# Performance work log

Hardware: AMD Instinct MI355X
Metric: run time of the kernel (lower is better)

The kernel has to match this reference:

```python
import jax, jax.numpy as jnp
import numpy as np

TOP_K = 2


def setup_inputs() -> dict:
    key = jax.random.key(0)
    ks = jax.random.split(key, 5)
    B, S, H, E, I = 2, 1024, 1024, 16, 1024
    scale = 1.0 / np.sqrt(H)
    return {
        "hidden_states": jax.random.normal(ks[0], (B, S, H), dtype=jnp.float32),
        "router_w": jax.random.normal(ks[1], (E, H), dtype=jnp.float32) * scale,   # nn.Linear(H,E).weight
        "gate_w": jax.random.normal(ks[2], (E, I, H), dtype=jnp.float32) * scale,  # per-expert Linear(H,I).weight
        "up_w": jax.random.normal(ks[3], (E, I, H), dtype=jnp.float32) * scale,
        "down_w": jax.random.normal(ks[4], (E, H, I), dtype=jnp.float32) * (1.0 / np.sqrt(I)),
    }


def reference(hidden_states, router_w, gate_w, up_w, down_w):
    orig_shape = hidden_states.shape
    x = hidden_states.reshape(-1, orig_shape[-1])  # [T, H]
    T = x.shape[0]
    E = router_w.shape[0]

    # Router: sigmoid -> top-k -> normalize
    logits = jnp.einsum("th,eh->te", x, router_w)           # [T, E]
    scores = jax.nn.sigmoid(logits)
    weights, indices = jax.lax.top_k(scores, TOP_K)         # [T, K]
    weights = weights / (weights.sum(axis=-1, keepdims=True) + 1e-20)

    # Dense per-token-per-expert combine weight (0 for unrouted pairs) ==
    # exact math of the torch gather/index_add loop.
    w_full = jnp.zeros((T, E), dtype=x.dtype).at[
        jnp.arange(T)[:, None], indices
    ].add(weights)                                          # [T, E]

    # Expert MLPs (SwiGLU) computed for all experts, zero-weighted combine.
    g = jax.nn.silu(jnp.einsum("th,eih->tei", x, gate_w))   # [T, E, I]
    u = jnp.einsum("th,eih->tei", x, up_w)                  # [T, E, I]
    out = jnp.einsum("te,tei,ehi->th", w_full, g * u, down_w)  # [T, H]
    return out.reshape(orig_shape)
```

## Files before the change

### kernel.cpp

```cpp
#include <hip/hip_runtime.h>
#include <stdint.h>

#define T_TOK 2048
#define H_DIM 1024
#define E_NUM 16
#define I_DIM 1024
#define TOTAL_ROWS (2 * T_TOK)
#define CPAD 16

typedef short bf16x8 __attribute__((ext_vector_type(8)));
typedef float f32x4 __attribute__((ext_vector_type(4)));

__device__ __forceinline__ void async_copy16(const void* g, void* l) {
  __builtin_amdgcn_global_load_lds(
      (const __attribute__((address_space(1))) void*)g,
      (__attribute__((address_space(3))) void*)l, 16, 0, 0);
}

__device__ __forceinline__ uint32_t f2bf(float f) {
  uint32_t u = __float_as_uint(f);
  return (u + 0x7FFFu + ((u >> 16) & 1u)) >> 16;
}
__device__ __forceinline__ uint32_t pk2bf(float lo, float hi) {
  return f2bf(lo) | (f2bf(hi) << 16);
}

__device__ __forceinline__ void stage8(const float* g, uint16_t* l) {
  float4 v0 = *(const float4*)g;
  float4 v1 = *(const float4*)(g + 4);
  uint4 p;
  p.x = pk2bf(v0.x, v0.y);
  p.y = pk2bf(v0.z, v0.w);
  p.z = pk2bf(v1.x, v1.y);
  p.w = pk2bf(v1.z, v1.w);
  *(uint4*)l = p;
}

__global__ __launch_bounds__(256) void router_kernel(
    const float* __restrict__ x, const float* __restrict__ rw,
    uint16_t* __restrict__ xbf, int* __restrict__ counts,
    int* __restrict__ tokens, float* __restrict__ wts) {
  const int t = blockIdx.x * 4 + (threadIdx.x >> 6);
  const int lane = threadIdx.x & 63;

  float4 xv[4];
  float acc[E_NUM];
#pragma unroll
  for (int e = 0; e < E_NUM; ++e) acc[e] = 0.f;

#pragma unroll
  for (int rep = 0; rep < 4; ++rep) {
    const int h0 = rep * 256 + lane * 4;
    xv[rep] = *(const float4*)(x + (size_t)t * H_DIM + h0);
    uint2 p;
    p.x = pk2bf(xv[rep].x, xv[rep].y);
    p.y = pk2bf(xv[rep].z, xv[rep].w);
    *(uint2*)(xbf + (size_t)t * H_DIM + h0) = p;
  }

#pragma unroll
  for (int e = 0; e < E_NUM; ++e) {
#pragma unroll
    for (int rep = 0; rep < 4; ++rep) {
      const float4 rv = *(const float4*)(rw + (size_t)e * H_DIM + rep * 256 + lane * 4);
      acc[e] += xv[rep].x * rv.x + xv[rep].y * rv.y + xv[rep].z * rv.z +
                xv[rep].w * rv.w;
    }
  }

#pragma unroll
  for (int e = 0; e < E_NUM; ++e) {
    float v = acc[e];
#pragma unroll
    for (int off = 32; off > 0; off >>= 1) v += __shfl_xor(v, off);
    acc[e] = v;
  }

  if (lane < 2) {
    float s[E_NUM];
#pragma unroll
    for (int e = 0; e < E_NUM; ++e) s[e] = 1.f / (1.f + expf(-acc[e]));
    int i1 = 0;
    float v1 = s[0];
#pragma unroll
    for (int e = 1; e < E_NUM; ++e)
      if (s[e] > v1) { v1 = s[e]; i1 = e; }
    int i2 = -1;
    float v2 = -1.f;
#pragma unroll
    for (int e = 0; e < E_NUM; ++e)
      if (e != i1 && s[e] > v2) { v2 = s[e]; i2 = e; }
    const float inv = 1.f / (v1 + v2 + 1e-20f);
    const int pe = (lane == 0) ? i1 : i2;
    const float pw = ((lane == 0) ? v1 : v2) * inv;
    const int slot = atomicAdd(&counts[pe * CPAD], 1);
    tokens[pe * T_TOK + slot] = t;
    wts[pe * T_TOK + slot] = pw;
  }
}

__global__ void offsets_kernel(const int* __restrict__ counts,
                               int* __restrict__ offsets) {
  if (threadIdx.x == 0) {
    int a = 0;
    for (int e = 0; e < E_NUM; ++e) {
      offsets[e] = a;
      a += counts[e * CPAD];
    }
    offsets[E_NUM] = a;
  }
}


__global__ __launch_bounds__(256, 4) void gemm1_kernel(
    const uint16_t* __restrict__ xbf, const float* __restrict__ gate,
    const float* __restrict__ up, const int* __restrict__ counts,
    const int* __restrict__ offsets, const int* __restrict__ tokens,
    const float* __restrict__ wts, uint16_t* __restrict__ hbuf) {
  const int e = blockIdx.z;
  const int count = counts[e * CPAD];
  const int m0 = blockIdx.y * 64;
  if (m0 >= count) return;
  const int n0 = blockIdx.x * 64;

  __shared__ __align__(16) uint16_t As[64 * 64];
  __shared__ __align__(16) uint16_t Bgs[64 * 64];
  __shared__ __align__(16) uint16_t Bus[64 * 64];
  __shared__ int tok_s[64];
  __shared__ float wt_s[64];

  const int tid = threadIdx.x;
  if (tid < 64) {
    const int slot = m0 + tid;
    int tk = 0;
    float w = 0.f;
    if (slot < count) {
      tk = tokens[e * T_TOK + slot];
      w = wts[e * T_TOK + slot];
    }
    tok_s[tid] = tk;
    wt_s[tid] = w;
  }
  __syncthreads();

  const int c0 = tid, c1 = tid + 256;
  const int m_a0 = c0 >> 3, m_a1 = c1 >> 3;
  const int kq0 = (c0 & 7) ^ (m_a0 & 7);
  const int kq1 = (c1 & 7) ^ (m_a1 & 7);

  const uint16_t* a_g0 = xbf + (size_t)tok_s[m_a0] * H_DIM + kq0 * 8;
  const uint16_t* a_g1 = xbf + (size_t)tok_s[m_a1] * H_DIM + kq1 * 8;
  uint16_t* a_l0 = As + c0 * 8;
  uint16_t* a_l1 = As + c1 * 8;

  const float* g_g0 = gate + ((size_t)e * I_DIM + n0 + m_a0) * H_DIM + kq0 * 8;
  const float* g_g1 = gate + ((size_t)e * I_DIM + n0 + m_a1) * H_DIM + kq1 * 8;
  const float* u_g0 = up + ((size_t)e * I_DIM + n0 + m_a0) * H_DIM + kq0 * 8;
  const float* u_g1 = up + ((size_t)e * I_DIM + n0 + m_a1) * H_DIM + kq1 * 8;
  uint16_t* bg_l0 = Bgs + c0 * 8;
  uint16_t* bg_l1 = Bgs + c1 * 8;
  uint16_t* bu_l0 = Bus + c0 * 8;
  uint16_t* bu_l1 = Bus + c1 * 8;

  const int wave = tid >> 6, lane = tid & 63;
  const int wm = (wave & 1) * 32, wn = (wave >> 1) * 32;
  const int lc = lane & 15, lq = lane >> 4;
  const int l7 = lc & 7;

  f32x4 accg[2][2], accu[2][2];
  const f32x4 zero4 = {0.f, 0.f, 0.f, 0.f};
#pragma unroll
  for (int i = 0; i < 2; ++i)
#pragma unroll
    for (int j = 0; j < 2; ++j) {
      accg[i][j] = zero4;
      accu[i][j] = zero4;
    }

  const int am[2] = {(wm + lc) * 64, (wm + 16 + lc) * 64};
  const int bn[2] = {(wn + lc) * 64, (wn + 16 + lc) * 64};

  for (int k0 = 0; k0 < H_DIM; k0 += 64) {
    __syncthreads();
    async_copy16(a_g0 + k0, a_l0);
    async_copy16(a_g1 + k0, a_l1);
    stage8(g_g0 + k0, bg_l0);
    stage8(g_g1 + k0, bg_l1);
    stage8(u_g0 + k0, bu_l0);
    stage8(u_g1 + k0, bu_l1);
    __syncthreads();

#pragma unroll
    for (int ks = 0; ks < 2; ++ks) {
      const int kswz = (((ks * 4 + lq) ^ l7)) * 8;
      bf16x8 af[2], bg[2], bu[2];
#pragma unroll
      for (int i = 0; i < 2; ++i) {
        af[i] = *(const bf16x8*)(As + am[i] + kswz);
        bg[i] = *(const bf16x8*)(Bgs + bn[i] + kswz);
        bu[i] = *(const bf16x8*)(Bus + bn[i] + kswz);
      }
#pragma unroll
      for (int im = 0; im < 2; ++im)
#pragma unroll
        for (int in = 0; in < 2; ++in) {
          accg[im][in] = __builtin_amdgcn_mfma_f32_16x16x32_bf16(
              af[im], bg[in], accg[im][in], 0, 0, 0);
          accu[im][in] = __builtin_amdgcn_mfma_f32_16x16x32_bf16(
              af[im], bu[in], accu[im][in], 0, 0, 0);
        }
    }
  }

  const int off_e = offsets[e];
#pragma unroll
  for (int im = 0; im < 2; ++im) {
#pragma unroll
    for (int r = 0; r < 4; ++r) {
      const int row = wm + im * 16 + lq * 4 + r;
      const int slot = m0 + row;
      if (slot < count) {
        const float w = wt_s[row];
        uint16_t* hrow = hbuf + (size_t)(off_e + slot) * I_DIM + n0 + wn;
#pragma unroll
        for (int in = 0; in < 2; ++in) {
          const float g = accg[im][in][r];
          const float u = accu[im][in][r];
          const float hv = g / (1.f + __expf(-g)) * u * w;
          hrow[in * 16 + lc] = (uint16_t)f2bf(hv);
        }
      }
    }
  }
}

__global__ __launch_bounds__(256, 4) void gemm2_kernel(
    const uint16_t* __restrict__ hbuf, const float* __restrict__ down,
    const int* __restrict__ counts, const int* __restrict__ offsets,
    const int* __restrict__ tokens, float* __restrict__ out) {
  const int e = blockIdx.z;
  const int count = counts[e * CPAD];
  const int m0 = blockIdx.y * 64;
  if (m0 >= count) return;
  const int n0 = blockIdx.x * 64;

  __shared__ __align__(16) uint16_t As[64 * 64];
  __shared__ __align__(16) uint16_t Bs[64 * 64];
  __shared__ int tok_s[64];

  const int tid = threadIdx.x;
  const int off_e = offsets[e];
  if (tid < 64) {
    const int slot = m0 + tid;
    tok_s[tid] = (slot < count) ? tokens[e * T_TOK + slot] : 0;
  }
  __syncthreads();

  const int c0 = tid, c1 = tid + 256;
  const int m_a0 = c0 >> 3, m_a1 = c1 >> 3;
  const int kq0 = (c0 & 7) ^ (m_a0 & 7);
  const int kq1 = (c1 & 7) ^ (m_a1 & 7);

  int r0 = off_e + m0 + m_a0;
  int r1 = off_e + m0 + m_a1;
  if (r0 > TOTAL_ROWS - 1) r0 = TOTAL_ROWS - 1;
  if (r1 > TOTAL_ROWS - 1) r1 = TOTAL_ROWS - 1;
  const uint16_t* a_g0 = hbuf + (size_t)r0 * I_DIM + kq0 * 8;
  const uint16_t* a_g1 = hbuf + (size_t)r1 * I_DIM + kq1 * 8;
  uint16_t* a_l0 = As + c0 * 8;
  uint16_t* a_l1 = As + c1 * 8;

  const float* d_g0 = down + ((size_t)e * H_DIM + n0 + m_a0) * I_DIM + kq0 * 8;
  const float* d_g1 = down + ((size_t)e * H_DIM + n0 + m_a1) * I_DIM + kq1 * 8;
  uint16_t* b_l0 = Bs + c0 * 8;
  uint16_t* b_l1 = Bs + c1 * 8;

  const int wave = tid >> 6, lane = tid & 63;
  const int wm = (wave & 1) * 32, wn = (wave >> 1) * 32;
  const int lc = lane & 15, lq = lane >> 4;
  const int l7 = lc & 7;

  f32x4 acc[2][2];
  const f32x4 zero4 = {0.f, 0.f, 0.f, 0.f};
#pragma unroll
  for (int i = 0; i < 2; ++i)
#pragma unroll
    for (int j = 0; j < 2; ++j) acc[i][j] = zero4;

  const int am[2] = {(wm + lc) * 64, (wm + 16 + lc) * 64};
  const int bn[2] = {(wn + lc) * 64, (wn + 16 + lc) * 64};

  for (int k0 = 0; k0 < I_DIM; k0 += 64) {
    __syncthreads();
    async_copy16(a_g0 + k0, a_l0);
    async_copy16(a_g1 + k0, a_l1);
    stage8(d_g0 + k0, b_l0);
    stage8(d_g1 + k0, b_l1);
    __syncthreads();

#pragma unroll
    for (int ks = 0; ks < 2; ++ks) {
      const int kswz = (((ks * 4 + lq) ^ l7)) * 8;
      bf16x8 af[2], bf[2];
#pragma unroll
      for (int i = 0; i < 2; ++i) {
        af[i] = *(const bf16x8*)(As + am[i] + kswz);
        bf[i] = *(const bf16x8*)(Bs + bn[i] + kswz);
      }
#pragma unroll
      for (int im = 0; im < 2; ++im)
#pragma unroll
        for (int in = 0; in < 2; ++in)
          acc[im][in] = __builtin_amdgcn_mfma_f32_16x16x32_bf16(
              af[im], bf[in], acc[im][in], 0, 0, 0);
    }
  }

#pragma unroll
  for (int im = 0; im < 2; ++im) {
#pragma unroll
    for (int r = 0; r < 4; ++r) {
      const int row = wm + im * 16 + lq * 4 + r;
      const int slot = m0 + row;
      if (slot < count) {
        float* orow = out + (size_t)tok_s[row] * H_DIM + n0 + wn;
#pragma unroll
        for (int in = 0; in < 2; ++in)
          atomicAdd(orow + in * 16 + lc, acc[im][in][r]);
      }
    }
  }
}

extern "C" void kernel_launch(void* const* d_in, const int* in_sizes, int n_in,
                              void* d_out, int out_size, void* d_ws,
                              size_t ws_size, hipStream_t stream) {
  const float* x = (const float*)d_in[0];
  const float* rw = (const float*)d_in[1];
  const float* gate = (const float*)d_in[2];
  const float* up = (const float*)d_in[3];
  const float* down = (const float*)d_in[4];
  float* out = (float*)d_out;

  uint8_t* ws = (uint8_t*)d_ws;
  int* counts = (int*)ws;
  int* offsets = (int*)(ws + 2048);
  int* tokens = (int*)(ws + 4096);
  float* wts = (float*)(ws + 4096 + 131072);
  uint16_t* xbf = (uint16_t*)(ws + 4096 + 262144);
  uint16_t* hbuf = (uint16_t*)(ws + 4096 + 262144 + 4194304);

  hipMemsetAsync(counts, 0, 2048, stream);
  hipMemsetAsync(out, 0, (size_t)out_size * sizeof(float), stream);

  router_kernel<<<512, 256, 0, stream>>>(x, rw, xbf, counts, tokens, wts);
  offsets_kernel<<<1, 64, 0, stream>>>(counts, offsets);
  gemm1_kernel<<<dim3(16, 32, 16), 256, 0, stream>>>(
      xbf, gate, up, counts, offsets, tokens, wts, hbuf);
  gemm2_kernel<<<dim3(16, 32, 16), 256, 0, stream>>>(hbuf, down, counts,
                                                     offsets, tokens, out);
}
```

Before: 300.7 us.

## Enlarge expert GEMM M-tile to 256 rows and prefetch fp32 weights into registers

Both expert GEMMs now use 512-thread blocks covering 256 token rows by 64 output columns instead of 64x64. This reuses each fp32 weight tile, which is converted to bf16 on the fly, across four times as many tokens, cutting redundant weight reads and conversions. The weight loads for the next k-step are issued into registers after the barrier so they overlap with the MFMA work. The cost is more LDS and registers per block, and more wasted rows for experts whose token count is not a multiple of 256.

Measured after the change: 285.0 us. 1.06x faster.

```diff
diff --git a/kernel.cpp b/kernel.cpp
--- a/kernel.cpp
+++ b/kernel.cpp
@@ -23,17 +23,6 @@
 }
 __device__ __forceinline__ uint32_t pk2bf(float lo, float hi) {
   return f2bf(lo) | (f2bf(hi) << 16);
-}
-
-__device__ __forceinline__ void stage8(const float* g, uint16_t* l) {
-  float4 v0 = *(const float4*)g;
-  float4 v1 = *(const float4*)(g + 4);
-  uint4 p;
-  p.x = pk2bf(v0.x, v0.y);
-  p.y = pk2bf(v0.z, v0.w);
-  p.z = pk2bf(v1.x, v1.y);
-  p.w = pk2bf(v1.z, v1.w);
-  *(uint4*)l = p;
 }
 
 __global__ __launch_bounds__(256) void router_kernel(
@@ -112,25 +101,25 @@
 }
 
 
-__global__ __launch_bounds__(256, 4) void gemm1_kernel(
+__global__ __launch_bounds__(512, 4) void gemm1_kernel(
     const uint16_t* __restrict__ xbf, const float* __restrict__ gate,
     const float* __restrict__ up, const int* __restrict__ counts,
     const int* __restrict__ offsets, const int* __restrict__ tokens,
     const float* __restrict__ wts, uint16_t* __restrict__ hbuf) {
   const int e = blockIdx.z;
   const int count = counts[e * CPAD];
-  const int m0 = blockIdx.y * 64;
+  const int m0 = blockIdx.y * 256;
   if (m0 >= count) return;
   const int n0 = blockIdx.x * 64;
 
-  __shared__ __align__(16) uint16_t As[64 * 64];
+  __shared__ __align__(16) uint16_t As[256 * 64];
   __shared__ __align__(16) uint16_t Bgs[64 * 64];
   __shared__ __align__(16) uint16_t Bus[64 * 64];
-  __shared__ int tok_s[64];
-  __shared__ float wt_s[64];
+  __shared__ int tok_s[256];
+  __shared__ float wt_s[256];
 
   const int tid = threadIdx.x;
-  if (tid < 64) {
+  if (tid < 256) {
     const int slot = m0 + tid;
     int tk = 0;
     float w = 0.f;
@@ -143,65 +132,85 @@
   }
   __syncthreads();
 
-  const int c0 = tid, c1 = tid + 256;
-  const int m_a0 = c0 >> 3, m_a1 = c1 >> 3;
-  const int kq0 = (c0 & 7) ^ (m_a0 & 7);
-  const int kq1 = (c1 & 7) ^ (m_a1 & 7);
-
-  const uint16_t* a_g0 = xbf + (size_t)tok_s[m_a0] * H_DIM + kq0 * 8;
-  const uint16_t* a_g1 = xbf + (size_t)tok_s[m_a1] * H_DIM + kq1 * 8;
-  uint16_t* a_l0 = As + c0 * 8;
-  uint16_t* a_l1 = As + c1 * 8;
-
-  const float* g_g0 = gate + ((size_t)e * I_DIM + n0 + m_a0) * H_DIM + kq0 * 8;
-  const float* g_g1 = gate + ((size_t)e * I_DIM + n0 + m_a1) * H_DIM + kq1 * 8;
-  const float* u_g0 = up + ((size_t)e * I_DIM + n0 + m_a0) * H_DIM + kq0 * 8;
-  const float* u_g1 = up + ((size_t)e * I_DIM + n0 + m_a1) * H_DIM + kq1 * 8;
-  uint16_t* bg_l0 = Bgs + c0 * 8;
-  uint16_t* bg_l1 = Bgs + c1 * 8;
-  uint16_t* bu_l0 = Bus + c0 * 8;
-  uint16_t* bu_l1 = Bus + c1 * 8;
+  const uint16_t* a_g[4];
+  uint16_t* a_l[4];
+#pragma unroll
+  for (int j = 0; j < 4; ++j) {
+    const int c = j * 512 + tid;
+    const int m = c >> 3;
+    const int kq = (c & 7) ^ (m & 7);
+    a_g[j] = xbf + (size_t)tok_s[m] * H_DIM + kq * 8;
+    a_l[j] = As + c * 8;
+  }
+  const int bm = tid >> 3;
+  const int bkq = (tid & 7) ^ (bm & 7);
+  const float* g_g = gate + ((size_t)e * I_DIM + n0 + bm) * H_DIM + bkq * 8;
+  const float* u_g = up + ((size_t)e * I_DIM + n0 + bm) * H_DIM + bkq * 8;
+  uint16_t* bg_l = Bgs + tid * 8;
+  uint16_t* bu_l = Bus + tid * 8;
 
   const int wave = tid >> 6, lane = tid & 63;
-  const int wm = (wave & 1) * 32, wn = (wave >> 1) * 32;
+  const int wm = (wave & 3) * 64, wn = (wave >> 2) * 32;
   const int lc = lane & 15, lq = lane >> 4;
   const int l7 = lc & 7;
 
-  f32x4 accg[2][2], accu[2][2];
+  f32x4 accg[4][2], accu[4][2];
   const f32x4 zero4 = {0.f, 0.f, 0.f, 0.f};
 #pragma unroll
-  for (int i = 0; i < 2; ++i)
+  for (int i = 0; i < 4; ++i)
 #pragma unroll
     for (int j = 0; j < 2; ++j) {
       accg[i][j] = zero4;
       accu[i][j] = zero4;
     }
 
-  const int am[2] = {(wm + lc) * 64, (wm + 16 + lc) * 64};
-  const int bn[2] = {(wn + lc) * 64, (wn + 16 + lc) * 64};
+  int am[4], bn[2];
+#pragma unroll
+  for (int i = 0; i < 4; ++i) am[i] = (wm + i * 16 + lc) * 64;
+#pragma unroll
+  for (int i = 0; i < 2; ++i) bn[i] = (wn + i * 16 + lc) * 64;
+
+  float4 gr0 = *(const float4*)g_g;
+  float4 gr1 = *(const float4*)(g_g + 4);
+  float4 ur0 = *(const float4*)u_g;
+  float4 ur1 = *(const float4*)(u_g + 4);
 
   for (int k0 = 0; k0 < H_DIM; k0 += 64) {
     __syncthreads();
-    async_copy16(a_g0 + k0, a_l0);
-    async_copy16(a_g1 + k0, a_l1);
-    stage8(g_g0 + k0, bg_l0);
-    stage8(g_g1 + k0, bg_l1);
-    stage8(u_g0 + k0, bu_l0);
-    stage8(u_g1 + k0, bu_l1);
+#pragma unroll
+    for (int j = 0; j < 4; ++j) async_copy16(a_g[j] + k0, a_l[j]);
+    uint4 p;
+    p.x = pk2bf(gr0.x, gr0.y);
+    p.y = pk2bf(gr0.z, gr0.w);
+    p.z = pk2bf(gr1.x, gr1.y);
+    p.w = pk2bf(gr1.z, gr1.w);
+    *(uint4*)bg_l = p;
+    p.x = pk2bf(ur0.x, ur0.y);
+    p.y = pk2bf(ur0.z, ur0.w);
+    p.z = pk2bf(ur1.x, ur1.y);
+    p.w = pk2bf(ur1.z, ur1.w);
+    *(uint4*)bu_l = p;
     __syncthreads();
+    if (k0 + 64 < H_DIM) {
+      gr0 = *(const float4*)(g_g + k0 + 64);
+      gr1 = *(const float4*)(g_g + k0 + 68);
+      ur0 = *(const float4*)(u_g + k0 + 64);
+      ur1 = *(const float4*)(u_g + k0 + 68);
+    }
 
 #pragma unroll
     for (int ks = 0; ks < 2; ++ks) {
-      const int kswz = (((ks * 4 + lq) ^ l7)) * 8;
-      bf16x8 af[2], bg[2], bu[2];
+      const int kswz = ((ks * 4 + lq) ^ l7) * 8;
+      bf16x8 af[4], bg[2], bu[2];
+#pragma unroll
+      for (int i = 0; i < 4; ++i) af[i] = *(const bf16x8*)(As + am[i] + kswz);
 #pragma unroll
       for (int i = 0; i < 2; ++i) {
-        af[i] = *(const bf16x8*)(As + am[i] + kswz);
         bg[i] = *(const bf16x8*)(Bgs + bn[i] + kswz);
         bu[i] = *(const bf16x8*)(Bus + bn[i] + kswz);
       }
 #pragma unroll
-      for (int im = 0; im < 2; ++im)
+      for (int im = 0; im < 4; ++im)
 #pragma unroll
         for (int in = 0; in < 2; ++in) {
           accg[im][in] = __builtin_amdgcn_mfma_f32_16x16x32_bf16(
@@ -214,7 +223,7 @@
 
   const int off_e = offsets[e];
 #pragma unroll
-  for (int im = 0; im < 2; ++im) {
+  for (int im = 0; im < 4; ++im) {
 #pragma unroll
     for (int r = 0; r < 4; ++r) {
       const int row = wm + im * 16 + lq * 4 + r;
@@ -234,81 +243,93 @@
   }
 }
 
-__global__ __launch_bounds__(256, 4) void gemm2_kernel(
+__global__ __launch_bounds__(512, 4) void gemm2_kernel(
     const uint16_t* __restrict__ hbuf, const float* __restrict__ down,
     const int* __restrict__ counts, const int* __restrict__ offsets,
     const int* __restrict__ tokens, float* __restrict__ out) {
   const int e = blockIdx.z;
   const int count = counts[e * CPAD];
-  const int m0 = blockIdx.y * 64;
+  const int m0 = blockIdx.y * 256;
   if (m0 >= count) return;
   const int n0 = blockIdx.x * 64;
 
-  __shared__ __align__(16) uint16_t As[64 * 64];
+  __shared__ __align__(16) uint16_t As[256 * 64];
   __shared__ __align__(16) uint16_t Bs[64 * 64];
-  __shared__ int tok_s[64];
+  __shared__ int tok_s[256];
 
   const int tid = threadIdx.x;
   const int off_e = offsets[e];
-  if (tid < 64) {
+  if (tid < 256) {
     const int slot = m0 + tid;
     tok_s[tid] = (slot < count) ? tokens[e * T_TOK + slot] : 0;
   }
-  __syncthreads();
-
-  const int c0 = tid, c1 = tid + 256;
-  const int m_a0 = c0 >> 3, m_a1 = c1 >> 3;
-  const int kq0 = (c0 & 7) ^ (m_a0 & 7);
-  const int kq1 = (c1 & 7) ^ (m_a1 & 7);
-
-  int r0 = off_e + m0 + m_a0;
-  int r1 = off_e + m0 + m_a1;
-  if (r0 > TOTAL_ROWS - 1) r0 = TOTAL_ROWS - 1;
-  if (r1 > TOTAL_ROWS - 1) r1 = TOTAL_ROWS - 1;
-  const uint16_t* a_g0 = hbuf + (size_t)r0 * I_DIM + kq0 * 8;
-  const uint16_t* a_g1 = hbuf + (size_t)r1 * I_DIM + kq1 * 8;
-  uint16_t* a_l0 = As + c0 * 8;
-  uint16_t* a_l1 = As + c1 * 8;
-
-  const float* d_g0 = down + ((size_t)e * H_DIM + n0 + m_a0) * I_DIM + kq0 * 8;
-  const float* d_g1 = down + ((size_t)e * H_DIM + n0 + m_a1) * I_DIM + kq1 * 8;
-  uint16_t* b_l0 = Bs + c0 * 8;
-  uint16_t* b_l1 = Bs + c1 * 8;
+
+  const uint16_t* a_g[4];
+  uint16_t* a_l[4];
+#pragma unroll
+  for (int j = 0; j < 4; ++j) {
+    const int c = j * 512 + tid;
+    const int m = c >> 3;
+    const int kq = (c & 7) ^ (m & 7);
+    int r = off_e + m0 + m;
+    if (r > TOTAL_ROWS - 1) r = TOTAL_ROWS - 1;
+    a_g[j] = hbuf + (size_t)r * I_DIM + kq * 8;
+    a_l[j] = As + c * 8;
+  }
+  const int bm = tid >> 3;
+  const int bkq = (tid & 7) ^ (bm & 7);
+  const float* d_g = down + ((size_t)e * H_DIM + n0 + bm) * I_DIM + bkq * 8;
+  uint16_t* b_l = Bs + tid * 8;
 
   const int wave = tid >> 6, lane = tid & 63;
-  const int wm = (wave & 1) * 32, wn = (wave >> 1) * 32;
+  const int wm = (wave & 3) * 64, wn = (wave >> 2) * 32;
   const int lc = lane & 15, lq = lane >> 4;
   const int l7 = lc & 7;
 
-  f32x4 acc[2][2];
+  f32x4 acc[4][2];
   const f32x4 zero4 = {0.f, 0.f, 0.f, 0.f};
 #pragma unroll
-  for (int i = 0; i < 2; ++i)
+  for (int i = 0; i < 4; ++i)
 #pragma unroll
     for (int j = 0; j < 2; ++j) acc[i][j] = zero4;
 
-  const int am[2] = {(wm + lc) * 64, (wm + 16 + lc) * 64};
-  const int bn[2] = {(wn + lc) * 64, (wn + 16 + lc) * 64};
+  int am[4], bn[2];
+#pragma unroll
+  for (int i = 0; i < 4; ++i) am[i] = (wm + i * 16 + lc) * 64;
+#pragma unroll
+  for (int i = 0; i < 2; ++i) bn[i] = (wn + i * 16 + lc) * 64;
+
+  __syncthreads();
+
+  float4 dr0 = *(const float4*)d_g;
+  float4 dr1 = *(const float4*)(d_g + 4);
 
   for (int k0 = 0; k0 < I_DIM; k0 += 64) {
     __syncthreads();
-    async_copy16(a_g0 + k0, a_l0);
-    async_copy16(a_g1 + k0, a_l1);
-    stage8(d_g0 + k0, b_l0);
-    stage8(d_g1 + k0, b_l1);
+#pragma unroll
+    for (int j = 0; j < 4; ++j) async_copy16(a_g[j] + k0, a_l[j]);
+    uint4 p;
+    p.x = pk2bf(dr0.x, dr0.y);
+    p.y = pk2bf(dr0.z, dr0.w);
+    p.z = pk2bf(dr1.x, dr1.y);
+    p.w = pk2bf(dr1.z, dr1.w);
+    *(uint4*)b_l = p;
     __syncthreads();
+    if (k0 + 64 < I_DIM) {
+      dr0 = *(const float4*)(d_g + k0 + 64);
+      dr1 = *(const float4*)(d_g + k0 + 68);
+    }
 
 #pragma unroll
     for (int ks = 0; ks < 2; ++ks) {
-      const int kswz = (((ks * 4 + lq) ^ l7)) * 8;
-      bf16x8 af[2], bf[2];
-#pragma unroll
-      for (int i = 0; i < 2; ++i) {
-        af[i] = *(const bf16x8*)(As + am[i] + kswz);
-        bf[i] = *(const bf16x8*)(Bs + bn[i] + kswz);
-      }
-#pragma unroll
-      for (int im = 0; im < 2; ++im)
+      const int kswz = ((ks * 4 + lq) ^ l7) * 8;
+      bf16x8 af[4], bf[2];
+#pragma unroll
+      for (int i = 0; i < 4; ++i) af[i] = *(const bf16x8*)(As + am[i] + kswz);
+#pragma unroll
+      for (int i = 0; i < 2; ++i) bf[i] = *(const bf16x8*)(Bs + bn[i] + kswz);
+#pragma unroll
+      for (int im = 0; im < 4; ++im)
 #pragma unroll
         for (int in = 0; in < 2; ++in)
           acc[im][in] = __builtin_amdgcn_mfma_f32_16x16x32_bf16(
@@ -317,7 +338,7 @@
   }
 
 #pragma unroll
-  for (int im = 0; im < 2; ++im) {
+  for (int im = 0; im < 4; ++im) {
 #pragma unroll
     for (int r = 0; r < 4; ++r) {
       const int row = wm + im * 16 + lq * 4 + r;
@@ -355,8 +376,8 @@
 
   router_kernel<<<512, 256, 0, stream>>>(x, rw, xbf, counts, tokens, wts);
   offsets_kernel<<<1, 64, 0, stream>>>(counts, offsets);
-  gemm1_kernel<<<dim3(16, 32, 16), 256, 0, stream>>>(
+  gemm1_kernel<<<dim3(16, 8, 16), 512, 0, stream>>>(
       xbf, gate, up, counts, offsets, tokens, wts, hbuf);
-  gemm2_kernel<<<dim3(16, 32, 16), 256, 0, stream>>>(hbuf, down, counts,
-                                                     offsets, tokens, out);
-}
+  gemm2_kernel<<<dim3(16, 8, 16), 512, 0, stream>>>(hbuf, down, counts,
+                                                    offsets, tokens, out);
+}
```
